# Performance work log

Hardware: AMD Instinct MI355X
Metric: run time of the kernel (lower is better)

## Reference

```python
import jax, jax.numpy as jnp
import numpy as np

DIMS, HEAD = 1024, 16
HD = DIMS // HEAD  # 64
MAX_ITER = 3
B, T = 4, 2048


def _ln(x, w, eps=1e-5):
    # torch LayerNorm with bias=False
    m = jnp.mean(x, axis=-1, keepdims=True)
    v = jnp.var(x, axis=-1, keepdims=True)
    return (x - m) * jax.lax.rsqrt(v + eps) * w


def setup_inputs() -> dict:
    key = jax.random.key(0)
    ks = jax.random.split(key, 10)
    n = lambda k, s: jax.random.normal(k, s, jnp.float32) * 0.02
    z = lambda s: jnp.zeros(s, jnp.float32)
    o = lambda s: jnp.ones(s, jnp.float32)
    return {
        "x": jax.random.normal(ks[0], (B, T, DIMS), jnp.float32),
        "Wq": n(ks[1], (DIMS, DIMS)), "bq": z((DIMS,)),
        "Wk": n(ks[2], (DIMS, DIMS)),
        "Wv": n(ks[3], (DIMS, DIMS)), "bv": z((DIMS,)),
        "Wo": n(ks[4], (DIMS, DIMS)), "bo": z((DIMS,)),
        "lna_w": o((DIMS,)), "lnc_w": o((HD,)), "lnd_w": o((HD,)),
        "Wlq": n(ks[5], (HD, HD)), "blq": z((HD,)),
        "Wlk": n(ks[6], (HD, HD)), "blk": z((HD,)),
        "Wlv": n(ks[7], (HD, HD)), "blv": z((HD,)),
        "temp": jnp.float32(1.0),
        "threshold": jnp.float32(0.01),
        "factor": jnp.float32(0.1),
    }


def reference(x, Wq, bq, Wk, Wv, bv, Wo, bo, lna_w, lnc_w, lnd_w,
              Wlq, blq, Wlk, blk, Wlv, blv, temp, threshold, factor):
    Bn, Tn, D = x.shape
    H, hd = HEAD, HD
    # .item() in torch detaches these params
    temp0 = jax.lax.stop_gradient(temp)
    thr = jax.lax.stop_gradient(threshold)
    fac = jax.lax.stop_gradient(factor)

    scale = hd ** -0.25
    xn = _ln(x, lna_w)
    q = (xn @ Wq.T + bq) * scale
    k = (xn @ Wk.T) * scale  # no bias
    v = xn @ Wv.T + bv
    shp = lambda t: t.reshape(Bn, Tn, H, hd).transpose(0, 2, 1, 3)  # (B,H,T,hd)
    q, k, v = shp(q), shp(k), shp(v)

    # eff_span = min(qcur.shape[1], k.shape[1]) == head dim of (B,H,T,hd)
    E = H
    sm_scale = 1.0 / float(np.sqrt(hd))

    qcur, kcur, vcur = q, k, v
    prev = jnp.zeros_like(q)
    attn_out = jnp.zeros_like(q)
    done = jnp.asarray(False)
    for it in range(MAX_ITER):
        ql = qcur[:, :, :E] @ Wlq.T + blq  # (B,H,E,hd)
        kl = kcur[:, :, :E] @ Wlk.T + blk
        vl = vcur[:, :, :E] @ Wlv.T + blv
        t_it = temp0 + 0.005 * it
        tscale = jnp.where((t_it != 1.0) & (t_it > 0), jax.lax.rsqrt(t_it), 1.0)
        qs = _ln(ql, lnc_w) * tscale
        ks_ = _ln(kl, lnd_w)
        logits = jnp.einsum('bhqd,bhkd->bhqk', qs, ks_) * sm_scale
        ai = jnp.einsum('bhqk,bhkd->bhqd', jax.nn.softmax(logits, axis=-1), vl)
        iter_out = jnp.zeros_like(qcur).at[:, :, :E].set(ai)
        diff = jnp.mean(jnp.abs(iter_out - prev))
        attn_out = jnp.where(done, attn_out, iter_out)  # freeze after break
        done = done | ((diff < thr + fac * diff) & (it > 0))
        prev = iter_out
        qcur = qcur + iter_out
        kcur, vcur = kl, vl

    out = attn_out.transpose(0, 2, 1, 3).reshape(Bn, Tn, D)
    return out @ Wo.T + bo
```

## Files before the change

kernel.cpp:

```cpp
#include <hip/hip_runtime.h>
#include <math.h>

#define WS_XN    0
#define WS_QKVP  65536
#define WS_DIFF  1638400
#define WS_AI1   1638404
#define WS_AI2   1703940
#define WS_WOP   1769476

__device__ __forceinline__ float4 f4zero() { return make_float4(0.f, 0.f, 0.f, 0.f); }
__device__ __forceinline__ float4 f4add(float4 a, float4 b) {
    return make_float4(a.x + b.x, a.y + b.y, a.z + b.z, a.w + b.w);
}
__device__ __forceinline__ float4 f4fma(float s, float4 a, float4 c) {
    return make_float4(fmaf(s, a.x, c.x), fmaf(s, a.y, c.y),
                       fmaf(s, a.z, c.z), fmaf(s, a.w, c.w));
}
__device__ __forceinline__ float dot4acc(float4 a, float4 b, float acc) {
    acc = fmaf(a.x, b.x, acc); acc = fmaf(a.y, b.y, acc);
    acc = fmaf(a.z, b.z, acc); acc = fmaf(a.w, b.w, acc);
    return acc;
}

__global__ __launch_bounds__(256) void k_ln(const float* __restrict__ x,
                                            const float* __restrict__ lna,
                                            float* __restrict__ xn,
                                            float* __restrict__ diffg) {
    int r = blockIdx.x;
    int b = r >> 4, t = r & 15;
    if (blockIdx.x == 0 && threadIdx.x == 0) diffg[0] = 0.f;
    const float* row = x + (size_t)(b * 2048 + t) * 1024;
    int tid = threadIdx.x;
    float4 xv = *(const float4*)&row[tid * 4];
    float s1 = xv.x + xv.y + xv.z + xv.w;
    float s2 = xv.x * xv.x + xv.y * xv.y + xv.z * xv.z + xv.w * xv.w;
    for (int off = 32; off; off >>= 1) {
        s1 += __shfl_xor(s1, off);
        s2 += __shfl_xor(s2, off);
    }
    __shared__ float ssum[4], ssq[4];
    int wv = tid >> 6, lane = tid & 63;
    if (lane == 0) { ssum[wv] = s1; ssq[wv] = s2; }
    __syncthreads();
    float tot = ssum[0] + ssum[1] + ssum[2] + ssum[3];
    float tq  = ssq[0] + ssq[1] + ssq[2] + ssq[3];
    float m   = tot * (1.0f / 1024.0f);
    float var = tq * (1.0f / 1024.0f) - m * m;
    float rs  = rsqrtf(var + 1e-5f);
    float4 w4 = *(const float4*)&lna[tid * 4];
    float4 o  = make_float4((xv.x - m) * rs * w4.x, (xv.y - m) * rs * w4.y,
                            (xv.z - m) * rs * w4.z, (xv.w - m) * rs * w4.w);
    *(float4*)&xn[r * 1024 + tid * 4] = o;
}

__global__ __launch_bounds__(256) void k_qkv(const float* __restrict__ xn,
                                             const float* __restrict__ Wq,
                                             const float* __restrict__ Wk,
                                             const float* __restrict__ Wv,
                                             float* __restrict__ qkvp) {
    int ct  = blockIdx.x;
    int ksl = blockIdx.y;
    int m   = ct >> 5;
    const float* W = (m == 0) ? Wq : (m == 1) ? Wk : Wv;
    int j0 = (ct & 31) * 32;
    int k0 = ksl * 128;
    __shared__ float At[64][132];
    __shared__ float Bt[32][132];
    int tid = threadIdx.x;
    for (int i = tid; i < 2048; i += 256) {
        int r = i >> 5, kk = (i & 31) << 2;
        *(float4*)&At[r][kk] = *(const float4*)&xn[r * 1024 + k0 + kk];
    }
    for (int i = tid; i < 1024; i += 256) {
        int r = i >> 5, kk = (i & 31) << 2;
        *(float4*)&Bt[r][kk] = *(const float4*)&W[(size_t)(j0 + r) * 1024 + k0 + kk];
    }
    __syncthreads();
    int rg = tid >> 4, cg = tid & 15;
    float acc[4][2];
#pragma unroll
    for (int i = 0; i < 4; i++) { acc[i][0] = 0.f; acc[i][1] = 0.f; }
    for (int k = 0; k < 128; k += 4) {
        float4 b0 = *(float4*)&Bt[cg * 2 + 0][k];
        float4 b1 = *(float4*)&Bt[cg * 2 + 1][k];
#pragma unroll
        for (int i = 0; i < 4; i++) {
            float4 a = *(float4*)&At[rg * 4 + i][k];
            acc[i][0] = dot4acc(a, b0, acc[i][0]);
            acc[i][1] = dot4acc(a, b1, acc[i][1]);
        }
    }
    float* dst = qkvp + (size_t)ksl * 196608;
    int colg = ct * 32 + cg * 2;
#pragma unroll
    for (int i = 0; i < 4; i++) {
        *(float2*)&dst[(rg * 4 + i) * 3072 + colg] = make_float2(acc[i][0], acc[i][1]);
    }
}

__global__ __launch_bounds__(256) void k_iter(
        const float* __restrict__ qkvp,
        const float* __restrict__ bq,  const float* __restrict__ bv,
        const float* __restrict__ lnc, const float* __restrict__ lnd,
        const float* __restrict__ Wlq, const float* __restrict__ blq,
        const float* __restrict__ Wlk, const float* __restrict__ blk_,
        const float* __restrict__ Wlv, const float* __restrict__ blv,
        const float* __restrict__ temp,
        float* __restrict__ ai1g, float* __restrict__ ai2g,
        float* __restrict__ diffg) {
    __shared__ float WA[4096];
    __shared__ float WB[4096];
    __shared__ float inq[16 * 68], ink[16 * 68], inv[16 * 68];
    __shared__ float qlS[16 * 68], klS[16 * 68], vlS[16 * 68];
    __shared__ float pS[16 * 17];
    __shared__ float dred[4];

    int tid  = threadIdx.x;
    int b    = blockIdx.x >> 4, h = blockIdx.x & 15;
    int t    = tid >> 4, dg = tid & 15;
    int lane = tid & 63, wv = tid >> 6;
    int rowi = b * 16 + t;
    int col  = h * 64 + dg * 4;

    for (int i = tid; i < 4096; i += 256) {
        int d = i >> 6, k = i & 63;
        WB[k * 64 + d] = Wlk[i];
    }

    const float SCALE = 0.35355339059327378f;
    float4 q4 = f4zero(), k4 = f4zero(), v4 = f4zero();
#pragma unroll
    for (int s = 0; s < 8; s++) {
        const float* P = qkvp + (size_t)s * 196608 + rowi * 3072 + col;
        q4 = f4add(q4, *(const float4*)&P[0]);
        k4 = f4add(k4, *(const float4*)&P[1024]);
        v4 = f4add(v4, *(const float4*)&P[2048]);
    }
    float4 bq4 = *(const float4*)&bq[col];
    float4 bv4 = *(const float4*)&bv[col];
    *(float4*)&inq[t * 68 + dg * 4] = make_float4(
        (q4.x + bq4.x) * SCALE, (q4.y + bq4.y) * SCALE,
        (q4.z + bq4.z) * SCALE, (q4.w + bq4.w) * SCALE);
    *(float4*)&ink[t * 68 + dg * 4] = make_float4(
        k4.x * SCALE, k4.y * SCALE, k4.z * SCALE, k4.w * SCALE);
    *(float4*)&inv[t * 68 + dg * 4] = f4add(v4, bv4);

    float4 blq4 = *(const float4*)&blq[dg * 4];
    float4 blk4 = *(const float4*)&blk_[dg * 4];
    float4 blv4 = *(const float4*)&blv[dg * 4];
    float lcw = lnc[lane], ldw = lnd[lane];
    float tempv = temp[0];

    float4 ai0 = f4zero(), ai1r = f4zero();
    float dlocal = 0.f;
    (void)ai1r;

    for (int it = 0; it < 3; ++it) {
        float t_it = tempv + 0.005f * (float)it;
        float tsc  = (t_it != 1.0f && t_it > 0.0f) ? rsqrtf(t_it) : 1.0f;

        for (int i = tid; i < 4096; i += 256) {
            int d = i >> 6, k = i & 63;
            WA[k * 64 + d] = Wlq[i];
        }
        __syncthreads();

        float4 aq = f4zero(), ak = f4zero();
        for (int k = 0; k < 64; ++k) {
            float qi = inq[t * 68 + k];
            float ki = ink[t * 68 + k];
            aq = f4fma(qi, *(float4*)&WA[k * 64 + dg * 4], aq);
            ak = f4fma(ki, *(float4*)&WB[k * 64 + dg * 4], ak);
        }
        aq = f4add(aq, blq4);
        ak = f4add(ak, blk4);
        *(float4*)&qlS[t * 68 + dg * 4] = aq;
        *(float4*)&klS[t * 68 + dg * 4] = ak;
        __syncthreads();

        for (int i = tid; i < 4096; i += 256) {
            int d = i >> 6, k = i & 63;
            WA[k * 64 + d] = Wlv[i];
        }
        float xq[4], xk[4], mq[4], rq[4], mk[4], rk[4];
#pragma unroll
        for (int s = 0; s < 4; ++s) {
            int tr = wv * 4 + s;
            xq[s] = qlS[tr * 68 + lane];
            xk[s] = klS[tr * 68 + lane];
            float s1q = xq[s], s2q = xq[s] * xq[s];
            float s1k = xk[s], s2k = xk[s] * xk[s];
            for (int off = 32; off; off >>= 1) {
                s1q += __shfl_xor(s1q, off); s2q += __shfl_xor(s2q, off);
                s1k += __shfl_xor(s1k, off); s2k += __shfl_xor(s2k, off);
            }
            mq[s] = s1q * (1.0f / 64.0f);
            float vq = s2q * (1.0f / 64.0f) - mq[s] * mq[s];
            rq[s] = rsqrtf(vq + 1e-5f);
            mk[s] = s1k * (1.0f / 64.0f);
            float vk = s2k * (1.0f / 64.0f) - mk[s] * mk[s];
            rk[s] = rsqrtf(vk + 1e-5f);
        }
        __syncthreads();
#pragma unroll
        for (int s = 0; s < 4; ++s) {
            int tr = wv * 4 + s;
            ink[tr * 68 + lane] = xk[s];
            qlS[tr * 68 + lane] = (xq[s] - mq[s]) * rq[s] * lcw * tsc;
            klS[tr * 68 + lane] = (xk[s] - mk[s]) * rk[s] * ldw;
        }
        __syncthreads();

        float acc = 0.f;
        for (int d = 0; d < 64; ++d)
            acc += qlS[t * 68 + d] * klS[dg * 68 + d];
        float lg = acc * 0.125f;
        float mx = lg;
        for (int off = 8; off; off >>= 1) mx = fmaxf(mx, __shfl_xor(mx, off));
        float e = expf(lg - mx);
        float sm = e;
        for (int off = 8; off; off >>= 1) sm += __shfl_xor(sm, off);
        pS[t * 17 + dg] = e / sm;
        __syncthreads();

        float4 av = f4zero();
        for (int k = 0; k < 64; ++k) {
            float vi = inv[t * 68 + k];
            av = f4fma(vi, *(float4*)&WA[k * 64 + dg * 4], av);
        }
        av = f4add(av, blv4);
        *(float4*)&vlS[t * 68 + dg * 4] = av;
        __syncthreads();

        float4 ai = f4zero();
#pragma unroll
        for (int jj = 0; jj < 16; ++jj)
            ai = f4fma(pS[t * 17 + jj], *(float4*)&vlS[jj * 68 + dg * 4], ai);

        if (it == 0) {
            ai0 = ai;
        } else if (it == 1) {
            dlocal = fabsf(ai.x - ai0.x) + fabsf(ai.y - ai0.y) +
                     fabsf(ai.z - ai0.z) + fabsf(ai.w - ai0.w);
            *(float4*)&ai1g[rowi * 1024 + col] = ai;
        } else {
            *(float4*)&ai2g[rowi * 1024 + col] = ai;
        }
        float4 q0 = *(float4*)&inq[t * 68 + dg * 4];
        *(float4*)&inq[t * 68 + dg * 4] = f4add(q0, ai);
        *(float4*)&inv[t * 68 + dg * 4] = av;
    }

    float ds = dlocal;
    for (int off = 32; off; off >>= 1) ds += __shfl_xor(ds, off);
    if (lane == 0) dred[wv] = ds;
    __syncthreads();
    if (tid == 0) atomicAdd(diffg, dred[0] + dred[1] + dred[2] + dred[3]);
}

__global__ __launch_bounds__(256) void k_wo(const float* __restrict__ ai1g,
                                            const float* __restrict__ ai2g,
                                            const float* __restrict__ diffg,
                                            const float* __restrict__ thrp,
                                            const float* __restrict__ facp,
                                            const float* __restrict__ Wo,
                                            float* __restrict__ wop) {
    float diff = diffg[0] * (1.0f / 8388608.0f);
    const float* A = (diff < thrp[0] + facp[0] * diff) ? ai1g : ai2g;
    int jt  = blockIdx.x;
    int ksl = blockIdx.y;
    int k0  = ksl * 128;
    __shared__ float At[64][132];
    __shared__ float Bt[32][132];
    int tid = threadIdx.x;
    for (int i = tid; i < 2048; i += 256) {
        int r = i >> 5, kk = (i & 31) << 2;
        *(float4*)&At[r][kk] = *(const float4*)&A[r * 1024 + k0 + kk];
    }
    for (int i = tid; i < 1024; i += 256) {
        int r = i >> 5, kk = (i & 31) << 2;
        *(float4*)&Bt[r][kk] = *(const float4*)&Wo[(size_t)(jt * 32 + r) * 1024 + k0 + kk];
    }
    __syncthreads();
    int rg = tid >> 4, cg = tid & 15;
    float acc[4][2];
#pragma unroll
    for (int i = 0; i < 4; i++) { acc[i][0] = 0.f; acc[i][1] = 0.f; }
    for (int k = 0; k < 128; k += 4) {
        float4 b0 = *(float4*)&Bt[cg * 2 + 0][k];
        float4 b1 = *(float4*)&Bt[cg * 2 + 1][k];
#pragma unroll
        for (int i = 0; i < 4; i++) {
            float4 a = *(float4*)&At[rg * 4 + i][k];
            acc[i][0] = dot4acc(a, b0, acc[i][0]);
            acc[i][1] = dot4acc(a, b1, acc[i][1]);
        }
    }
    float* dst = wop + (size_t)ksl * 65536;
    int colg = jt * 32 + cg * 2;
#pragma unroll
    for (int i = 0; i < 4; i++) {
        *(float2*)&dst[(rg * 4 + i) * 1024 + colg] = make_float2(acc[i][0], acc[i][1]);
    }
}

__global__ __launch_bounds__(256) void k_bo(const float* __restrict__ bo,
                                            const float* __restrict__ wop,
                                            float* __restrict__ out) {
    int row = blockIdx.x;
    int tid = threadIdx.x;
    int b = row >> 11, t = row & 2047;
    float4 o = *(const float4*)&bo[tid * 4];
    if (t < 16) {
        int ri = b * 16 + t;
#pragma unroll
        for (int s = 0; s < 8; s++) {
            float4 p = *(const float4*)&wop[(size_t)s * 65536 + ri * 1024 + tid * 4];
            o = f4add(o, p);
        }
    }
    *(float4*)&out[(size_t)row * 1024 + tid * 4] = o;
}

extern "C" void kernel_launch(void* const* d_in, const int* in_sizes, int n_in,
                              void* d_out, int out_size, void* d_ws, size_t ws_size,
                              hipStream_t stream) {
    (void)in_sizes; (void)n_in; (void)out_size; (void)ws_size;
    const float* x    = (const float*)d_in[0];
    const float* Wq   = (const float*)d_in[1];
    const float* bq   = (const float*)d_in[2];
    const float* Wk   = (const float*)d_in[3];
    const float* Wv   = (const float*)d_in[4];
    const float* bv   = (const float*)d_in[5];
    const float* Wo   = (const float*)d_in[6];
    const float* bo   = (const float*)d_in[7];
    const float* lna  = (const float*)d_in[8];
    const float* lnc  = (const float*)d_in[9];
    const float* lnd  = (const float*)d_in[10];
    const float* Wlq  = (const float*)d_in[11];
    const float* blq  = (const float*)d_in[12];
    const float* Wlk  = (const float*)d_in[13];
    const float* blk_ = (const float*)d_in[14];
    const float* Wlv  = (const float*)d_in[15];
    const float* blv  = (const float*)d_in[16];
    const float* temp = (const float*)d_in[17];
    const float* thr  = (const float*)d_in[18];
    const float* fac  = (const float*)d_in[19];
    float* ws  = (float*)d_ws;
    float* out = (float*)d_out;

    k_ln  <<<64, 256, 0, stream>>>(x, lna, ws + WS_XN, ws + WS_DIFF);
    k_qkv <<<dim3(96, 8), 256, 0, stream>>>(ws + WS_XN, Wq, Wk, Wv, ws + WS_QKVP);
    k_iter<<<64, 256, 0, stream>>>(ws + WS_QKVP, bq, bv, lnc, lnd,
                                   Wlq, blq, Wlk, blk_, Wlv, blv, temp,
                                   ws + WS_AI1, ws + WS_AI2, ws + WS_DIFF);
    k_wo  <<<dim3(32, 8), 256, 0, stream>>>(ws + WS_AI1, ws + WS_AI2, ws + WS_DIFF,
                                            thr, fac, Wo, ws + WS_WOP);
    k_bo  <<<8192, 256, 0, stream>>>(bo, ws + WS_WOP, out);
}
```

Baseline: 178.3 us.

## Restructure iteration kernel with pretransposed weights and per-wave register-tiled projections

Measured after the change: 183.1 us. 2.7% more time.

```diff
diff --git a/kernel.cpp b/kernel.cpp
--- a/kernel.cpp
+++ b/kernel.cpp
@@ -7,6 +7,7 @@
 #define WS_AI1   1638404
 #define WS_AI2   1703940
 #define WS_WOP   1769476
+#define WS_WT    2293764
 
 __device__ __forceinline__ float4 f4zero() { return make_float4(0.f, 0.f, 0.f, 0.f); }
 __device__ __forceinline__ float4 f4add(float4 a, float4 b) {
@@ -24,8 +25,22 @@
 
 __global__ __launch_bounds__(256) void k_ln(const float* __restrict__ x,
                                             const float* __restrict__ lna,
+                                            const float* __restrict__ Wlq,
+                                            const float* __restrict__ Wlk,
+                                            const float* __restrict__ Wlv,
                                             float* __restrict__ xn,
+                                            float* __restrict__ wt,
                                             float* __restrict__ diffg) {
+    if (blockIdx.x >= 64) {
+        int m = blockIdx.x - 64;
+        const float* W = (m == 0) ? Wlq : (m == 1) ? Wlk : Wlv;
+        float* dst = wt + m * 4096;
+        for (int i = threadIdx.x; i < 4096; i += 256) {
+            int k = i >> 6, d = i & 63;
+            dst[i] = W[d * 64 + k];
+        }
+        return;
+    }
     int r = blockIdx.x;
     int b = r >> 4, t = r & 15;
     if (blockIdx.x == 0 && threadIdx.x == 0) diffg[0] = 0.f;
@@ -99,156 +114,227 @@
 }
 
 __global__ __launch_bounds__(256) void k_iter(
-        const float* __restrict__ qkvp,
+        const float* __restrict__ qkvp, const float* __restrict__ wt,
         const float* __restrict__ bq,  const float* __restrict__ bv,
         const float* __restrict__ lnc, const float* __restrict__ lnd,
-        const float* __restrict__ Wlq, const float* __restrict__ blq,
-        const float* __restrict__ Wlk, const float* __restrict__ blk_,
-        const float* __restrict__ Wlv, const float* __restrict__ blv,
-        const float* __restrict__ temp,
+        const float* __restrict__ blq, const float* __restrict__ blk_,
+        const float* __restrict__ blv, const float* __restrict__ temp,
         float* __restrict__ ai1g, float* __restrict__ ai2g,
         float* __restrict__ diffg) {
-    __shared__ float WA[4096];
-    __shared__ float WB[4096];
-    __shared__ float inq[16 * 68], ink[16 * 68], inv[16 * 68];
-    __shared__ float qlS[16 * 68], klS[16 * 68], vlS[16 * 68];
-    __shared__ float pS[16 * 17];
+    __shared__ __align__(16) float qcT[64 * 20];
+    __shared__ __align__(16) float kcT[64 * 20];
+    __shared__ __align__(16) float vcT[64 * 20];
+    __shared__ __align__(16) float qsR[16 * 68];
+    __shared__ __align__(16) float ksR[16 * 68];
+    __shared__ __align__(16) float vlR[16 * 68];
     __shared__ float dred[4];
 
     int tid  = threadIdx.x;
     int b    = blockIdx.x >> 4, h = blockIdx.x & 15;
-    int t    = tid >> 4, dg = tid & 15;
-    int lane = tid & 63, wv = tid >> 6;
-    int rowi = b * 16 + t;
-    int col  = h * 64 + dg * 4;
-
-    for (int i = tid; i < 4096; i += 256) {
-        int d = i >> 6, k = i & 63;
-        WB[k * 64 + d] = Wlk[i];
-    }
-
-    const float SCALE = 0.35355339059327378f;
-    float4 q4 = f4zero(), k4 = f4zero(), v4 = f4zero();
-#pragma unroll
-    for (int s = 0; s < 8; s++) {
-        const float* P = qkvp + (size_t)s * 196608 + rowi * 3072 + col;
-        q4 = f4add(q4, *(const float4*)&P[0]);
-        k4 = f4add(k4, *(const float4*)&P[1024]);
-        v4 = f4add(v4, *(const float4*)&P[2048]);
-    }
-    float4 bq4 = *(const float4*)&bq[col];
-    float4 bv4 = *(const float4*)&bv[col];
-    *(float4*)&inq[t * 68 + dg * 4] = make_float4(
-        (q4.x + bq4.x) * SCALE, (q4.y + bq4.y) * SCALE,
-        (q4.z + bq4.z) * SCALE, (q4.w + bq4.w) * SCALE);
-    *(float4*)&ink[t * 68 + dg * 4] = make_float4(
-        k4.x * SCALE, k4.y * SCALE, k4.z * SCALE, k4.w * SCALE);
-    *(float4*)&inv[t * 68 + dg * 4] = f4add(v4, bv4);
-
-    float4 blq4 = *(const float4*)&blq[dg * 4];
-    float4 blk4 = *(const float4*)&blk_[dg * 4];
-    float4 blv4 = *(const float4*)&blv[dg * 4];
-    float lcw = lnc[lane], ldw = lnd[lane];
+    int wv   = tid >> 6, lane = tid & 63;
     float tempv = temp[0];
 
-    float4 ai0 = f4zero(), ai1r = f4zero();
-    float dlocal = 0.f;
-    (void)ai1r;
+    {
+        int t = tid >> 4, dg = tid & 15;
+        int rowi = b * 16 + t, col = h * 64 + dg * 4;
+        const float SCALE = 0.35355339059327378f;
+        float4 q4 = f4zero(), k4 = f4zero(), v4 = f4zero();
+#pragma unroll
+        for (int s = 0; s < 8; s++) {
+            const float* P = qkvp + (size_t)s * 196608 + rowi * 3072 + col;
+            q4 = f4add(q4, *(const float4*)&P[0]);
+            k4 = f4add(k4, *(const float4*)&P[1024]);
+            v4 = f4add(v4, *(const float4*)&P[2048]);
+        }
+        float4 bq4 = *(const float4*)&bq[col];
+        float4 bv4 = *(const float4*)&bv[col];
+        float qv[4] = { (q4.x + bq4.x) * SCALE, (q4.y + bq4.y) * SCALE,
+                        (q4.z + bq4.z) * SCALE, (q4.w + bq4.w) * SCALE };
+        float kv[4] = { k4.x * SCALE, k4.y * SCALE, k4.z * SCALE, k4.w * SCALE };
+        float vv[4] = { v4.x + bv4.x, v4.y + bv4.y, v4.z + bv4.z, v4.w + bv4.w };
+#pragma unroll
+        for (int c = 0; c < 4; c++) {
+            qcT[(dg * 4 + c) * 20 + t] = qv[c];
+            kcT[(dg * 4 + c) * 20 + t] = kv[c];
+            vcT[(dg * 4 + c) * 20 + t] = vv[c];
+        }
+    }
+    __syncthreads();
+
+    int tq = lane >> 4, dq = lane & 15;
+    int t2 = tid >> 4,  u  = tid & 15;
+    int rowi2 = b * 16 + t2, col2 = h * 64 + u * 4;
+
+    float4 ai0 = f4zero();
+    float  dlocal = 0.f;
 
     for (int it = 0; it < 3; ++it) {
         float t_it = tempv + 0.005f * (float)it;
         float tsc  = (t_it != 1.0f && t_it > 0.0f) ? rsqrtf(t_it) : 1.0f;
 
-        for (int i = tid; i < 4096; i += 256) {
-            int d = i >> 6, k = i & 63;
-            WA[k * 64 + d] = Wlq[i];
+        if (wv == 0) {
+            const float* WT = wt;
+            float acc[4][4];
+#pragma unroll
+            for (int i = 0; i < 4; i++)
+#pragma unroll
+                for (int j = 0; j < 4; j++) acc[i][j] = 0.f;
+#pragma unroll 8
+            for (int k = 0; k < 64; ++k) {
+                float4 a4 = *(float4*)&qcT[k * 20 + 4 * tq];
+                float4 b4 = *(const float4*)&WT[k * 64 + 4 * dq];
+                float av[4] = { a4.x, a4.y, a4.z, a4.w };
+#pragma unroll
+                for (int i = 0; i < 4; i++) {
+                    acc[i][0] = fmaf(av[i], b4.x, acc[i][0]);
+                    acc[i][1] = fmaf(av[i], b4.y, acc[i][1]);
+                    acc[i][2] = fmaf(av[i], b4.z, acc[i][2]);
+                    acc[i][3] = fmaf(av[i], b4.w, acc[i][3]);
+                }
+            }
+            float4 bb = *(const float4*)&blq[4 * dq];
+            float4 lw = *(const float4*)&lnc[4 * dq];
+#pragma unroll
+            for (int i = 0; i < 4; i++) {
+                acc[i][0] += bb.x; acc[i][1] += bb.y;
+                acc[i][2] += bb.z; acc[i][3] += bb.w;
+                float s1 = acc[i][0] + acc[i][1] + acc[i][2] + acc[i][3];
+                float s2 = acc[i][0]*acc[i][0] + acc[i][1]*acc[i][1]
+                         + acc[i][2]*acc[i][2] + acc[i][3]*acc[i][3];
+                for (int off = 8; off; off >>= 1) {
+                    s1 += __shfl_xor(s1, off); s2 += __shfl_xor(s2, off);
+                }
+                float m  = s1 * (1.0f / 64.0f);
+                float vr = s2 * (1.0f / 64.0f) - m * m;
+                float rs = rsqrtf(vr + 1e-5f) * tsc;
+                float4 o = make_float4((acc[i][0] - m) * rs * lw.x,
+                                       (acc[i][1] - m) * rs * lw.y,
+                                       (acc[i][2] - m) * rs * lw.z,
+                                       (acc[i][3] - m) * rs * lw.w);
+                *(float4*)&qsR[(4 * tq + i) * 68 + 4 * dq] = o;
+            }
+        } else if (wv == 1) {
+            const float* WT = wt + 4096;
+            float acc[4][4];
+#pragma unroll
+            for (int i = 0; i < 4; i++)
+#pragma unroll
+                for (int j = 0; j < 4; j++) acc[i][j] = 0.f;
+#pragma unroll 8
+            for (int k = 0; k < 64; ++k) {
+                float4 a4 = *(float4*)&kcT[k * 20 + 4 * tq];
+                float4 b4 = *(const float4*)&WT[k * 64 + 4 * dq];
+                float av[4] = { a4.x, a4.y, a4.z, a4.w };
+#pragma unroll
+                for (int i = 0; i < 4; i++) {
+                    acc[i][0] = fmaf(av[i], b4.x, acc[i][0]);
+                    acc[i][1] = fmaf(av[i], b4.y, acc[i][1]);
+                    acc[i][2] = fmaf(av[i], b4.z, acc[i][2]);
+                    acc[i][3] = fmaf(av[i], b4.w, acc[i][3]);
+                }
+            }
+            float4 bb = *(const float4*)&blk_[4 * dq];
+#pragma unroll
+            for (int i = 0; i < 4; i++) {
+                acc[i][0] += bb.x; acc[i][1] += bb.y;
+                acc[i][2] += bb.z; acc[i][3] += bb.w;
+            }
+#pragma unroll
+            for (int j = 0; j < 4; j++) {
+                float4 cv = make_float4(acc[0][j], acc[1][j], acc[2][j], acc[3][j]);
+                *(float4*)&kcT[(4 * dq + j) * 20 + 4 * tq] = cv;
+            }
+            float4 lw = *(const float4*)&lnd[4 * dq];
+#pragma unroll
+            for (int i = 0; i < 4; i++) {
+                float s1 = acc[i][0] + acc[i][1] + acc[i][2] + acc[i][3];
+                float s2 = acc[i][0]*acc[i][0] + acc[i][1]*acc[i][1]
+                         + acc[i][2]*acc[i][2] + acc[i][3]*acc[i][3];
+                for (int off = 8; off; off >>= 1) {
+                    s1 += __shfl_xor(s1, off); s2 += __shfl_xor(s2, off);
+                }
+                float m  = s1 * (1.0f / 64.0f);
+                float vr = s2 * (1.0f / 64.0f) - m * m;
+                float rs = rsqrtf(vr + 1e-5f);
+                float4 o = make_float4((acc[i][0] - m) * rs * lw.x,
+                                       (acc[i][1] - m) * rs * lw.y,
+                                       (acc[i][2] - m) * rs * lw.z,
+                                       (acc[i][3] - m) * rs * lw.w);
+                *(float4*)&ksR[(4 * tq + i) * 68 + 4 * dq] = o;
+            }
+        } else if (wv == 2) {
+            const float* WT = wt + 8192;
+            float acc[4][4];
+#pragma unroll
+            for (int i = 0; i < 4; i++)
+#pragma unroll
+                for (int j = 0; j < 4; j++) acc[i][j] = 0.f;
+#pragma unroll 8
+            for (int k = 0; k < 64; ++k) {
+                float4 a4 = *(float4*)&vcT[k * 20 + 4 * tq];
+                float4 b4 = *(const float4*)&WT[k * 64 + 4 * dq];
+                float av[4] = { a4.x, a4.y, a4.z, a4.w };
+#pragma unroll
+                for (int i = 0; i < 4; i++) {
+                    acc[i][0] = fmaf(av[i], b4.x, acc[i][0]);
+                    acc[i][1] = fmaf(av[i], b4.y, acc[i][1]);
+                    acc[i][2] = fmaf(av[i], b4.z, acc[i][2]);
+                    acc[i][3] = fmaf(av[i], b4.w, acc[i][3]);
+                }
+            }
+            float4 bb = *(const float4*)&blv[4 * dq];
+#pragma unroll
+            for (int i = 0; i < 4; i++) {
+                acc[i][0] += bb.x; acc[i][1] += bb.y;
+                acc[i][2] += bb.z; acc[i][3] += bb.w;
+                *(float4*)&vlR[(4 * tq + i) * 68 + 4 * dq] =
+                    make_float4(acc[i][0], acc[i][1], acc[i][2], acc[i][3]);
+            }
+#pragma unroll
+            for (int j = 0; j < 4; j++) {
+                float4 cv = make_float4(acc[0][j], acc[1][j], acc[2][j], acc[3][j]);
+                *(float4*)&vcT[(4 * dq + j) * 20 + 4 * tq] = cv;
+            }
         }
         __syncthreads();
 
-        float4 aq = f4zero(), ak = f4zero();
-        for (int k = 0; k < 64; ++k) {
-            float qi = inq[t * 68 + k];
-            float ki = ink[t * 68 + k];
-            aq = f4fma(qi, *(float4*)&WA[k * 64 + dg * 4], aq);
-            ak = f4fma(ki, *(float4*)&WB[k * 64 + dg * 4], ak);
-        }
-        aq = f4add(aq, blq4);
-        ak = f4add(ak, blk4);
-        *(float4*)&qlS[t * 68 + dg * 4] = aq;
-        *(float4*)&klS[t * 68 + dg * 4] = ak;
-        __syncthreads();
-
-        for (int i = tid; i < 4096; i += 256) {
-            int d = i >> 6, k = i & 63;
-            WA[k * 64 + d] = Wlv[i];
-        }
-        float xq[4], xk[4], mq[4], rq[4], mk[4], rk[4];
-#pragma unroll
-        for (int s = 0; s < 4; ++s) {
-            int tr = wv * 4 + s;
-            xq[s] = qlS[tr * 68 + lane];
-            xk[s] = klS[tr * 68 + lane];
-            float s1q = xq[s], s2q = xq[s] * xq[s];
-            float s1k = xk[s], s2k = xk[s] * xk[s];
-            for (int off = 32; off; off >>= 1) {
-                s1q += __shfl_xor(s1q, off); s2q += __shfl_xor(s2q, off);
-                s1k += __shfl_xor(s1k, off); s2k += __shfl_xor(s2k, off);
-            }
-            mq[s] = s1q * (1.0f / 64.0f);
-            float vq = s2q * (1.0f / 64.0f) - mq[s] * mq[s];
-            rq[s] = rsqrtf(vq + 1e-5f);
-            mk[s] = s1k * (1.0f / 64.0f);
-            float vk = s2k * (1.0f / 64.0f) - mk[s] * mk[s];
-            rk[s] = rsqrtf(vk + 1e-5f);
-        }
-        __syncthreads();
-#pragma unroll
-        for (int s = 0; s < 4; ++s) {
-            int tr = wv * 4 + s;
-            ink[tr * 68 + lane] = xk[s];
-            qlS[tr * 68 + lane] = (xq[s] - mq[s]) * rq[s] * lcw * tsc;
-            klS[tr * 68 + lane] = (xk[s] - mk[s]) * rk[s] * ldw;
-        }
-        __syncthreads();
-
-        float acc = 0.f;
-        for (int d = 0; d < 64; ++d)
-            acc += qlS[t * 68 + d] * klS[dg * 68 + d];
-        float lg = acc * 0.125f;
+        float lg = 0.f;
+#pragma unroll
+        for (int c = 0; c < 16; ++c) {
+            float4 a4 = *(float4*)&qsR[t2 * 68 + 4 * c];
+            float4 b4 = *(float4*)&ksR[u  * 68 + 4 * c];
+            lg = dot4acc(a4, b4, lg);
+        }
+        lg *= 0.125f;
         float mx = lg;
         for (int off = 8; off; off >>= 1) mx = fmaxf(mx, __shfl_xor(mx, off));
-        float e = expf(lg - mx);
+        float e = __expf(lg - mx);
         float sm = e;
         for (int off = 8; off; off >>= 1) sm += __shfl_xor(sm, off);
-        pS[t * 17 + dg] = e / sm;
-        __syncthreads();
-
-        float4 av = f4zero();
-        for (int k = 0; k < 64; ++k) {
-            float vi = inv[t * 68 + k];
-            av = f4fma(vi, *(float4*)&WA[k * 64 + dg * 4], av);
-        }
-        av = f4add(av, blv4);
-        *(float4*)&vlS[t * 68 + dg * 4] = av;
-        __syncthreads();
+        float p = e / sm;
 
         float4 ai = f4zero();
-#pragma unroll
-        for (int jj = 0; jj < 16; ++jj)
-            ai = f4fma(pS[t * 17 + jj], *(float4*)&vlS[jj * 68 + dg * 4], ai);
+        int gbase = lane & 48;
+#pragma unroll
+        for (int tk = 0; tk < 16; ++tk) {
+            float pk = __shfl(p, gbase + tk);
+            ai = f4fma(pk, *(float4*)&vlR[tk * 68 + 4 * u], ai);
+        }
 
         if (it == 0) {
             ai0 = ai;
         } else if (it == 1) {
             dlocal = fabsf(ai.x - ai0.x) + fabsf(ai.y - ai0.y) +
                      fabsf(ai.z - ai0.z) + fabsf(ai.w - ai0.w);
-            *(float4*)&ai1g[rowi * 1024 + col] = ai;
+            *(float4*)&ai1g[rowi2 * 1024 + col2] = ai;
         } else {
-            *(float4*)&ai2g[rowi * 1024 + col] = ai;
-        }
-        float4 q0 = *(float4*)&inq[t * 68 + dg * 4];
-        *(float4*)&inq[t * 68 + dg * 4] = f4add(q0, ai);
-        *(float4*)&inv[t * 68 + dg * 4] = av;
+            *(float4*)&ai2g[rowi2 * 1024 + col2] = ai;
+        }
+        qcT[(4 * u + 0) * 20 + t2] += ai.x;
+        qcT[(4 * u + 1) * 20 + t2] += ai.y;
+        qcT[(4 * u + 2) * 20 + t2] += ai.z;
+        qcT[(4 * u + 3) * 20 + t2] += ai.w;
+        __syncthreads();
     }
 
     float ds = dlocal;
@@ -349,10 +435,11 @@
     float* ws  = (float*)d_ws;
     float* out = (float*)d_out;
 
-    k_ln  <<<64, 256, 0, stream>>>(x, lna, ws + WS_XN, ws + WS_DIFF);
+    k_ln  <<<67, 256, 0, stream>>>(x, lna, Wlq, Wlk, Wlv,
+                                   ws + WS_XN, ws + WS_WT, ws + WS_DIFF);
     k_qkv <<<dim3(96, 8), 256, 0, stream>>>(ws + WS_XN, Wq, Wk, Wv, ws + WS_QKVP);
-    k_iter<<<64, 256, 0, stream>>>(ws + WS_QKVP, bq, bv, lnc, lnd,
-                                   Wlq, blq, Wlk, blk_, Wlv, blv, temp,
+    k_iter<<<64, 256, 0, stream>>>(ws + WS_QKVP, ws + WS_WT, bq, bv, lnc, lnd,
+                                   blq, blk_, blv, temp,
                                    ws + WS_AI1, ws + WS_AI2, ws + WS_DIFF);
     k_wo  <<<dim3(32, 8), 256, 0, stream>>>(ws + WS_AI1, ws + WS_AI2, ws + WS_DIFF,
                                             thr, fac, Wo, ws + WS_WOP);
```
